# Kernel tuning notes

Measured on AMD Instinct MI355X. Metric: run time of the kernel, lower is better.

The kernel has to match this reference:

```python
import jax, jax.numpy as jnp
import numpy as np

MODEL_BATCHES = 2048
NUM_POINTS = 8192
N_FUNCS = 8
REMOVE_ITERS = 51  # remove_points = 51 * model_batches -> first 51 iterations dropped


def setup_inputs() -> dict:
    key = jax.random.key(0)
    k1, k2, k3, k4, k5 = jax.random.split(key, 5)
    point = jax.random.normal(k1, (MODEL_BATCHES, 2, 1), dtype=jnp.float32) * 0.1
    optimized_weights = jax.random.normal(k2, (N_FUNCS, 2, 2), dtype=jnp.float32) * 0.5
    optimized_biases = jax.random.normal(k3, (N_FUNCS, 2, 1), dtype=jnp.float32) * 0.5
    optimized_function_ops = jax.random.uniform(k4, (N_FUNCS,), dtype=jnp.float32)
    index = jax.random.randint(k5, (MODEL_BATCHES, NUM_POINTS), 0, N_FUNCS, dtype=jnp.int32)
    return {
        "point": point,
        "optimized_weights": optimized_weights,
        "optimized_biases": optimized_biases,
        "optimized_function_ops": optimized_function_ops,
        "index": index,
    }


def reference(point, optimized_weights, optimized_biases, optimized_function_ops, index):
    mb = point.shape[0]

    def step(p, idx):  # p: [mb,2,1], idx: [mb]
        W = optimized_weights[idx]          # [mb,2,2]
        b = optimized_biases[idx]           # [mb,2,1]
        op = optimized_function_ops[idx]    # [mb]
        p_new = jnp.einsum('bij,bjk->bik', W, p) + b  # [mb,2,1]
        out = jnp.concatenate([p_new[:, :, 0], op[:, None]], axis=1)  # [mb,3]
        return p_new, out

    # scan over iterations: index.T is [num_points, mb]
    _, outs = jax.lax.scan(step, point, index.T)  # outs: [num_points, mb, 3]
    pts = outs.reshape(-1, 3)  # matches torch.cat along dim 0 then squeeze
    return pts[REMOVE_ITERS * mb:, :]
```

## Files before the change

### kernel.cpp

```cpp
#include <hip/hip_runtime.h>

#define MB   2048
#define NP   8192
#define NF   8
#define RM   51
#define NCH  64
#define CH   128
#define SEG  32
#define NSEG 4

#define ELEM(v, s) ( (((s) & 3) == 0) ? (v)[(s) >> 2].x \
                   : (((s) & 3) == 1) ? (v)[(s) >> 2].y \
                   : (((s) & 3) == 2) ? (v)[(s) >> 2].z \
                   :                    (v)[(s) >> 2].w )


__global__ __launch_bounds__(256) void ifs_phase1(
    const int* __restrict__ idxg, const float* __restrict__ W,
    const float* __restrict__ B, float4* __restrict__ maps)
{
    __shared__ __align__(16) float4 pA[64];
    __shared__ __align__(16) float2 pC[64];
    const int tid = threadIdx.x;
    if (tid < 64) {
        const int fb = tid & 7;
        const int fa = tid >> 3;
        const float wa00 = W[fa*4+0], wa01 = W[fa*4+1], wa10 = W[fa*4+2], wa11 = W[fa*4+3];
        const float wb00 = W[fb*4+0], wb01 = W[fb*4+1], wb10 = W[fb*4+2], wb11 = W[fb*4+3];
        const float ba0 = B[fa*2+0], ba1 = B[fa*2+1];
        const float bb0 = B[fb*2+0], bb1 = B[fb*2+1];
        pA[tid] = make_float4(wa00*wb00 + wa01*wb10, wa00*wb01 + wa01*wb11,
                              wa10*wb00 + wa11*wb10, wa10*wb01 + wa11*wb11);
        pC[tid] = make_float2(wa00*bb0 + wa01*bb1 + ba0,
                              wa10*bb0 + wa11*bb1 + ba1);
    }
    __syncthreads();

    const int c = blockIdx.x >> 3;
    const int b = ((blockIdx.x & 7) << 8) + tid;
    const int4* ip = (const int4*)(idxg + (size_t)b * NP + c * CH);

    int4 va[8], vb[8];
    #pragma unroll
    for (int k = 0; k < 8; ++k) va[k] = ip[k];

    float a00 = 1.f, a01 = 0.f, a10 = 0.f, a11 = 1.f, c0 = 0.f, c1 = 0.f;

    for (int seg = 0; seg < NSEG; ++seg) {
        if (seg + 1 < NSEG) {
            #pragma unroll
            for (int k = 0; k < 8; ++k) vb[k] = ip[(seg + 1) * 8 + k];
        }
        #pragma unroll
        for (int s = 0; s < SEG; s += 2) {
            const int e = ELEM(va, s + 1) * 8 + ELEM(va, s);
            const float4 P = pA[e];
            const float2 q = pC[e];
            const float na00 = P.x*a00 + P.y*a10;
            const float na01 = P.x*a01 + P.y*a11;
            const float na10 = P.z*a00 + P.w*a10;
            const float na11 = P.z*a01 + P.w*a11;
            const float nc0  = P.x*c0  + P.y*c1 + q.x;
            const float nc1  = P.z*c0  + P.w*c1 + q.y;
            a00 = na00; a01 = na01; a10 = na10; a11 = na11; c0 = nc0; c1 = nc1;
        }
        #pragma unroll
        for (int k = 0; k < 8; ++k) va[k] = vb[k];
    }
    const size_t n = ((size_t)c * MB + b) * 2;
    maps[n]     = make_float4(a00, a01, a10, a11);
    maps[n + 1] = make_float4(c0,  c1,  0.f, 0.f);
}

__global__ __launch_bounds__(256) void ifs_phase2(
    const float2* __restrict__ point, const float4* __restrict__ maps,
    float2* __restrict__ pe)
{
    const int b = blockIdx.x * 256 + threadIdx.x;
    float2 p = point[b];
    float4 lo[8], hi[8], nlo[8], nhi[8];
    #pragma unroll
    for (int k = 0; k < 8; ++k) {
        lo[k] = maps[((size_t)k * MB + b) * 2];
        hi[k] = maps[((size_t)k * MB + b) * 2 + 1];
    }
    for (int g = 0; g < 8; ++g) {
        if (g < 7) {
            #pragma unroll
            for (int k = 0; k < 8; ++k) {
                nlo[k] = maps[((size_t)((g + 1) * 8 + k) * MB + b) * 2];
                nhi[k] = maps[((size_t)((g + 1) * 8 + k) * MB + b) * 2 + 1];
            }
        }
        #pragma unroll
        for (int k = 0; k < 8; ++k) {
            pe[(size_t)(g * 8 + k) * MB + b] = p;
            const float nx = lo[k].x * p.x + lo[k].y * p.y + hi[k].x;
            const float ny = lo[k].z * p.x + lo[k].w * p.y + hi[k].y;
            p.x = nx; p.y = ny;
        }
        #pragma unroll
        for (int k = 0; k < 8; ++k) { lo[k] = nlo[k]; hi[k] = nhi[k]; }
    }
}

template <bool CHECK>
__device__ __forceinline__ void phase3_body(
    const int4* ip, const float4* tA, const float4* tB,
    float2 p, float* o, int c)
{
    int4 va[8], vb[8];
    #pragma unroll
    for (int k = 0; k < 8; ++k) va[k] = ip[k];

    for (int seg = 0; seg < NSEG; ++seg) {
        if (seg + 1 < NSEG) {
            #pragma unroll
            for (int k = 0; k < 8; ++k) vb[k] = ip[(seg + 1) * 8 + k];
        }
        #pragma unroll
        for (int s = 0; s < SEG; ++s) {
            const int f = ELEM(va, s);
            const float4 w  = tA[f];
            const float4 bb = tB[f];
            const float nx = w.x * p.x + w.y * p.y + bb.x;
            const float ny = w.z * p.x + w.w * p.y + bb.y;
            p.x = nx; p.y = ny;
            if (!CHECK || (seg * SEG + s) >= RM) {
                o[0] = p.x; o[1] = p.y; o[2] = bb.z;
            }
            o += MB * 3;
        }
        #pragma unroll
        for (int k = 0; k < 8; ++k) va[k] = vb[k];
    }
}

__global__ __launch_bounds__(256) void ifs_phase3(
    const int* __restrict__ idxg, const float* __restrict__ W,
    const float* __restrict__ B, const float* __restrict__ OPS,
    const float2* __restrict__ pe, float* __restrict__ out)
{
    __shared__ __align__(16) float4 tA[NF];
    __shared__ __align__(16) float4 tB[NF];
    const int tid = threadIdx.x;
    if (tid < NF) {
        tA[tid] = make_float4(W[tid*4+0], W[tid*4+1], W[tid*4+2], W[tid*4+3]);
        tB[tid] = make_float4(B[tid*2+0], B[tid*2+1], OPS[tid], 0.f);
    }
    __syncthreads();

    const int c = blockIdx.x >> 3;
    const int b = ((blockIdx.x & 7) << 8) + tid;
    const int4* ip = (const int4*)(idxg + (size_t)b * NP + c * CH);

    const float2 p = pe[(size_t)c * MB + b];
    float* o = out + ((long long)c * CH - RM) * (MB * 3) + (long long)b * 3;

    if (c == 0) phase3_body<true >(ip, tA, tB, p, o, c);
    else        phase3_body<false>(ip, tA, tB, p, o, c);
}

extern "C" void kernel_launch(void* const* d_in, const int* in_sizes, int n_in,
                              void* d_out, int out_size, void* d_ws, size_t ws_size,
                              hipStream_t stream) {
    const float* point = (const float*)d_in[0];
    const float* W     = (const float*)d_in[1];
    const float* B     = (const float*)d_in[2];
    const float* OPS   = (const float*)d_in[3];
    const int*   idx   = (const int*)  d_in[4];
    float*       out   = (float*)d_out;

    float*  ws   = (float*)d_ws;
    float4* maps = (float4*)ws;
    float2* pe   = (float2*)(ws + (size_t)NCH * MB * 8);

    ifs_phase1<<<NCH * (MB / 256), 256, 0, stream>>>(idx, W, B, maps);
    ifs_phase2<<<MB / 256, 256, 0, stream>>>((const float2*)point, maps, pe);
    ifs_phase3<<<NCH * (MB / 256), 256, 0, stream>>>(idx, W, B, OPS, pe, out);
}
```

Baseline: 77.99 us.

## Stage index tiles through LDS for coalesced loads, split phase3 launch, nontemporal stores

Phase1 and phase3 now load the index matrix cooperatively into an LDS tile, so consecutive lanes read consecutive addresses, and each thread then reads its own row from LDS. Before, each thread strided through its own row in global memory. Phase1 also stores the pair products in SoA LDS arrays. Phase3 is split into two template launches so the first-chunk check is resolved at compile time, and its output writes use nontemporal stores. This adds LDS traffic, __syncthreads barriers and one extra kernel launch, and lowers occupancy because of the larger shared memory use.

```diff
diff --git a/kernel.cpp b/kernel.cpp
--- a/kernel.cpp
+++ b/kernel.cpp
@@ -6,68 +6,58 @@
 #define RM   51
 #define NCH  64
 #define CH   128
-#define SEG  32
-#define NSEG 4
-
-#define ELEM(v, s) ( (((s) & 3) == 0) ? (v)[(s) >> 2].x \
-                   : (((s) & 3) == 1) ? (v)[(s) >> 2].y \
-                   : (((s) & 3) == 2) ? (v)[(s) >> 2].z \
-                   :                    (v)[(s) >> 2].w )
 
 
 __global__ __launch_bounds__(256) void ifs_phase1(
     const int* __restrict__ idxg, const float* __restrict__ W,
     const float* __restrict__ B, float4* __restrict__ maps)
 {
-    __shared__ __align__(16) float4 pA[64];
-    __shared__ __align__(16) float2 pC[64];
+    __shared__ int tile[256][35];
+    __shared__ float P00[64], P01[64], P10[64], P11[64], Q0[64], Q1[64];
     const int tid = threadIdx.x;
     if (tid < 64) {
         const int fb = tid & 7;
         const int fa = tid >> 3;
         const float wa00 = W[fa*4+0], wa01 = W[fa*4+1], wa10 = W[fa*4+2], wa11 = W[fa*4+3];
         const float wb00 = W[fb*4+0], wb01 = W[fb*4+1], wb10 = W[fb*4+2], wb11 = W[fb*4+3];
-        const float ba0 = B[fa*2+0], ba1 = B[fa*2+1];
-        const float bb0 = B[fb*2+0], bb1 = B[fb*2+1];
-        pA[tid] = make_float4(wa00*wb00 + wa01*wb10, wa00*wb01 + wa01*wb11,
-                              wa10*wb00 + wa11*wb10, wa10*wb01 + wa11*wb11);
-        pC[tid] = make_float2(wa00*bb0 + wa01*bb1 + ba0,
-                              wa10*bb0 + wa11*bb1 + ba1);
+        P00[tid] = wa00*wb00 + wa01*wb10;  P01[tid] = wa00*wb01 + wa01*wb11;
+        P10[tid] = wa10*wb00 + wa11*wb10;  P11[tid] = wa10*wb01 + wa11*wb11;
+        Q0[tid]  = wa00*B[fb*2+0] + wa01*B[fb*2+1] + B[fa*2+0];
+        Q1[tid]  = wa10*B[fb*2+0] + wa11*B[fb*2+1] + B[fa*2+1];
     }
-    __syncthreads();
 
-    const int c = blockIdx.x >> 3;
-    const int b = ((blockIdx.x & 7) << 8) + tid;
-    const int4* ip = (const int4*)(idxg + (size_t)b * NP + c * CH);
-
-    int4 va[8], vb[8];
-    #pragma unroll
-    for (int k = 0; k < 8; ++k) va[k] = ip[k];
+    const int c   = blockIdx.x >> 3;
+    const int b0  = (blockIdx.x & 7) << 8;
+    const int x16 = tid & 15, yy = tid >> 4;
 
     float a00 = 1.f, a01 = 0.f, a10 = 0.f, a11 = 1.f, c0 = 0.f, c1 = 0.f;
 
-    for (int seg = 0; seg < NSEG; ++seg) {
-        if (seg + 1 < NSEG) {
-            #pragma unroll
-            for (int k = 0; k < 8; ++k) vb[k] = ip[(seg + 1) * 8 + k];
+    for (int seg = 0; seg < 2; ++seg) {
+        const int tb = c * CH + seg * 64;
+        #pragma unroll
+        for (int p = 0; p < 16; ++p) {
+            const int row = yy + p * 16;
+            const int4 v = *(const int4*)(idxg + (size_t)(b0 + row) * NP + tb + x16 * 4);
+            tile[row][x16*2+0] = v.y * 8 + v.x;
+            tile[row][x16*2+1] = v.w * 8 + v.z;
         }
+        __syncthreads();
         #pragma unroll
-        for (int s = 0; s < SEG; s += 2) {
-            const int e = ELEM(va, s + 1) * 8 + ELEM(va, s);
-            const float4 P = pA[e];
-            const float2 q = pC[e];
-            const float na00 = P.x*a00 + P.y*a10;
-            const float na01 = P.x*a01 + P.y*a11;
-            const float na10 = P.z*a00 + P.w*a10;
-            const float na11 = P.z*a01 + P.w*a11;
-            const float nc0  = P.x*c0  + P.y*c1 + q.x;
-            const float nc1  = P.z*c0  + P.w*c1 + q.y;
+        for (int j = 0; j < 32; ++j) {
+            const int e = tile[tid][j];
+            const float p00 = P00[e], p01 = P01[e], p10 = P10[e], p11 = P11[e];
+            const float q0 = Q0[e], q1 = Q1[e];
+            const float na00 = p00*a00 + p01*a10;
+            const float na01 = p00*a01 + p01*a11;
+            const float na10 = p10*a00 + p11*a10;
+            const float na11 = p10*a01 + p11*a11;
+            const float nc0  = p00*c0  + p01*c1 + q0;
+            const float nc1  = p10*c0  + p11*c1 + q1;
             a00 = na00; a01 = na01; a10 = na10; a11 = na11; c0 = nc0; c1 = nc1;
         }
-        #pragma unroll
-        for (int k = 0; k < 8; ++k) va[k] = vb[k];
+        __syncthreads();
     }
-    const size_t n = ((size_t)c * MB + b) * 2;
+    const size_t n = ((size_t)c * MB + b0 + tid) * 2;
     maps[n]     = make_float4(a00, a01, a10, a11);
     maps[n + 1] = make_float4(c0,  c1,  0.f, 0.f);
 }
@@ -105,42 +95,29 @@
 }
 
 template <bool CHECK>
-__device__ __forceinline__ void phase3_body(
-    const int4* ip, const float4* tA, const float4* tB,
-    float2 p, float* o, int c)
+__device__ __forceinline__ void phase3_step(
+    int f, const float4* tA, const float4* tB, float2& p, float*& o, int t_loc)
 {
-    int4 va[8], vb[8];
-    #pragma unroll
-    for (int k = 0; k < 8; ++k) va[k] = ip[k];
-
-    for (int seg = 0; seg < NSEG; ++seg) {
-        if (seg + 1 < NSEG) {
-            #pragma unroll
-            for (int k = 0; k < 8; ++k) vb[k] = ip[(seg + 1) * 8 + k];
-        }
-        #pragma unroll
-        for (int s = 0; s < SEG; ++s) {
-            const int f = ELEM(va, s);
-            const float4 w  = tA[f];
-            const float4 bb = tB[f];
-            const float nx = w.x * p.x + w.y * p.y + bb.x;
-            const float ny = w.z * p.x + w.w * p.y + bb.y;
-            p.x = nx; p.y = ny;
-            if (!CHECK || (seg * SEG + s) >= RM) {
-                o[0] = p.x; o[1] = p.y; o[2] = bb.z;
-            }
-            o += MB * 3;
-        }
-        #pragma unroll
-        for (int k = 0; k < 8; ++k) va[k] = vb[k];
+    const float4 w  = tA[f];
+    const float4 bb = tB[f];
+    const float nx = w.x * p.x + w.y * p.y + bb.x;
+    const float ny = w.z * p.x + w.w * p.y + bb.y;
+    p.x = nx; p.y = ny;
+    if (!CHECK || t_loc >= RM) {
+        __builtin_nontemporal_store(p.x,  o + 0);
+        __builtin_nontemporal_store(p.y,  o + 1);
+        __builtin_nontemporal_store(bb.z, o + 2);
     }
+    o += MB * 3;
 }
 
+template <bool CHECK>
 __global__ __launch_bounds__(256) void ifs_phase3(
     const int* __restrict__ idxg, const float* __restrict__ W,
     const float* __restrict__ B, const float* __restrict__ OPS,
     const float2* __restrict__ pe, float* __restrict__ out)
 {
+    __shared__ int tile[256][36];
     __shared__ __align__(16) float4 tA[NF];
     __shared__ __align__(16) float4 tB[NF];
     const int tid = threadIdx.x;
@@ -148,17 +125,34 @@
         tA[tid] = make_float4(W[tid*4+0], W[tid*4+1], W[tid*4+2], W[tid*4+3]);
         tB[tid] = make_float4(B[tid*2+0], B[tid*2+1], OPS[tid], 0.f);
     }
-    __syncthreads();
 
-    const int c = blockIdx.x >> 3;
-    const int b = ((blockIdx.x & 7) << 8) + tid;
-    const int4* ip = (const int4*)(idxg + (size_t)b * NP + c * CH);
+    const int c  = CHECK ? 0 : (blockIdx.x >> 3) + 1;
+    const int b0 = (blockIdx.x & 7) << 8;
+    const int b  = b0 + tid;
+    const int x4 = tid & 7, yy = tid >> 3;
 
-    const float2 p = pe[(size_t)c * MB + b];
+    float2 p = pe[(size_t)c * MB + b];
     float* o = out + ((long long)c * CH - RM) * (MB * 3) + (long long)b * 3;
 
-    if (c == 0) phase3_body<true >(ip, tA, tB, p, o, c);
-    else        phase3_body<false>(ip, tA, tB, p, o, c);
+    for (int seg = 0; seg < 4; ++seg) {
+        const int tb = c * CH + seg * 32;
+        #pragma unroll
+        for (int p8 = 0; p8 < 8; ++p8) {
+            const int row = yy + p8 * 32;
+            *(int4*)&tile[row][x4*4] = *(const int4*)(idxg + (size_t)(b0 + row) * NP + tb + x4 * 4);
+        }
+        __syncthreads();
+        #pragma unroll
+        for (int g = 0; g < 8; ++g) {
+            const int4 f4 = *(const int4*)&tile[tid][g*4];
+            const int base = seg * 32 + g * 4;
+            phase3_step<CHECK>(f4.x, tA, tB, p, o, base + 0);
+            phase3_step<CHECK>(f4.y, tA, tB, p, o, base + 1);
+            phase3_step<CHECK>(f4.z, tA, tB, p, o, base + 2);
+            phase3_step<CHECK>(f4.w, tA, tB, p, o, base + 3);
+        }
+        __syncthreads();
+    }
 }
 
 extern "C" void kernel_launch(void* const* d_in, const int* in_sizes, int n_in,
@@ -177,5 +171,6 @@
 
     ifs_phase1<<<NCH * (MB / 256), 256, 0, stream>>>(idx, W, B, maps);
     ifs_phase2<<<MB / 256, 256, 0, stream>>>((const float2*)point, maps, pe);
-    ifs_phase3<<<NCH * (MB / 256), 256, 0, stream>>>(idx, W, B, OPS, pe, out);
+    ifs_phase3<true ><<<1 * (MB / 256), 256, 0, stream>>>(idx, W, B, OPS, pe, out);
+    ifs_phase3<false><<<(NCH - 1) * (MB / 256), 256, 0, stream>>>(idx, W, B, OPS, pe, out);
 }
```

Measured after the change: 82.12 us. 5.3% more time.
